# Optimization experiments

Hardware: AMD Instinct MI355X
Metric: run time of the kernel (lower is better)

## Reference

```python
import jax, jax.numpy as jnp
import numpy as np

EPS = 1e-12  # F.normalize eps

def _l2norm(x):
    n = jnp.linalg.norm(x, axis=-1, keepdims=True)
    return x / jnp.maximum(n, EPS)

def setup_inputs() -> dict:
    key = jax.random.key(0)
    k1, k2, k3, k4 = jax.random.split(key, 4)
    N, D = 16384, 256
    img = jax.random.normal(k1, (N, D), dtype=jnp.float32)
    txt = jax.random.normal(k2, (N, D), dtype=jnp.float32)
    t_prime = jax.random.normal(k3, (), dtype=jnp.float32)
    bias = jax.random.normal(k4, (), dtype=jnp.float32)
    return {"img": img, "txt": txt, "t_prime": t_prime, "bias": bias}

def reference(img, txt, t_prime, bias):
    # world_size == 1 path of DistributedSigLoss.forward
    n = img.shape[0]
    image_features = _l2norm(img)
    text_features = _l2norm(txt)
    # logits = exp(t') * img @ txt.T + b   -> [N, N]
    logits = jnp.exp(t_prime) * (image_features @ text_features.T) + bias
    # labels = 2*I - 1 (positive pairs on the diagonal, negatives elsewhere)
    labels = 2.0 * jnp.eye(n, dtype=logits.dtype) - 1.0
    loss = -jnp.sum(jax.nn.log_sigmoid(labels * logits)) / n
    return loss
```

## Files before the change

### kernel.cpp

```cpp
#include <hip/hip_runtime.h>

typedef int   i32x4 __attribute__((ext_vector_type(4)));
typedef int   i32x8 __attribute__((ext_vector_type(8)));
typedef float f32x16 __attribute__((ext_vector_type(16)));

#define D_DIM 256
#define LOG2E 1.4426950408889634f
#define LN2   0.6931471805599453f
#define STRIP_BYTES 32768
#define NBLK 16384

#if __has_builtin(__builtin_amdgcn_exp2f)
static __device__ __forceinline__ float exp2_fast(float x) { return __builtin_amdgcn_exp2f(x); }
#else
static __device__ __forceinline__ float exp2_fast(float x) { return __expf(x * LN2); }
#endif
#if __has_builtin(__builtin_amdgcn_logf)
static __device__ __forceinline__ float log2_fast(float x) { return __builtin_amdgcn_logf(x); }
#else
static __device__ __forceinline__ float log2_fast(float x) { return __logf(x) * LOG2E; }
#endif

#if __has_builtin(__builtin_amdgcn_cvt_pk_fp8_f32)
static __device__ __forceinline__ unsigned int pack4_fp8(float a, float b, float c, float d) {
    int v = 0;
    v = __builtin_amdgcn_cvt_pk_fp8_f32(a, b, v, false);
    v = __builtin_amdgcn_cvt_pk_fp8_f32(c, d, v, true);
    return (unsigned int)v;
}
#else
#include <hip/hip_fp8.h>
static __device__ __forceinline__ unsigned char cv1(float x) {
    __hip_fp8_e4m3 f(x);
    union { __hip_fp8_e4m3 f; unsigned char b; } u; u.f = f; return u.b;
}
static __device__ __forceinline__ unsigned int pack4_fp8(float a, float b, float c, float d) {
    return (unsigned int)cv1(a) | ((unsigned int)cv1(b) << 8) |
           ((unsigned int)cv1(c) << 16) | ((unsigned int)cv1(d) << 24);
}
#endif

static __device__ __forceinline__ f32x16 mfma_fp8_32x32_k64(i32x8 a, i32x8 b, f32x16 c) {
#if __has_builtin(__builtin_amdgcn_mfma_scale_f32_32x32x64_f8f6f4)
    return __builtin_amdgcn_mfma_scale_f32_32x32x64_f8f6f4(a, b, c, 0, 0, 0, 127, 0, 127);
#else
    union { i32x8 v; long l[4]; } ua, ub;
    ua.v = a; ub.v = b;
#pragma unroll
    for (int s = 0; s < 4; ++s)
        c = __builtin_amdgcn_mfma_f32_32x32x16_fp8_fp8(ua.l[s], ub.l[s], c, 0, 0, 0);
    return c;
#endif
}

__global__ __launch_bounds__(256) void norm_cast_kernel(
    const float* __restrict__ img, const float* __restrict__ txt,
    unsigned char* __restrict__ Ab, unsigned char* __restrict__ Bb, int N)
{
    const int tid = threadIdx.x;
    const int q   = tid & 3;
    const int rl  = tid >> 2;
    int gRow = blockIdx.x * 64 + rl;

    const float* src;
    unsigned char* dstB;
    int row;
    if (gRow < N) { row = gRow;     src = img + (size_t)row * D_DIM; dstB = Ab; }
    else          { row = gRow - N; src = txt + (size_t)row * D_DIM; dstB = Bb; }

    float f[64];
    float ss = 0.0f;
    const float4* s4 = (const float4*)(src + q * 64);
#pragma unroll
    for (int i = 0; i < 16; ++i) {
        float4 v = s4[i];
        f[4*i+0] = v.x; f[4*i+1] = v.y; f[4*i+2] = v.z; f[4*i+3] = v.w;
        ss += v.x*v.x + v.y*v.y + v.z*v.z + v.w*v.w;
    }
    ss += __shfl_xor(ss, 1, 64);
    ss += __shfl_xor(ss, 2, 64);
    float inv = 1.0f / fmaxf(sqrtf(ss), 1e-12f);

    unsigned char* dst = dstB + (size_t)(row >> 7) * STRIP_BYTES + (row & 127) * 16;
#pragma unroll
    for (int g = 0; g < 4; ++g) {
        const float* h = f + g * 16;
        uint4 w;
        w.x = pack4_fp8(h[ 0]*inv, h[ 1]*inv, h[ 2]*inv, h[ 3]*inv);
        w.y = pack4_fp8(h[ 4]*inv, h[ 5]*inv, h[ 6]*inv, h[ 7]*inv);
        w.z = pack4_fp8(h[ 8]*inv, h[ 9]*inv, h[10]*inv, h[11]*inv);
        w.w = pack4_fp8(h[12]*inv, h[13]*inv, h[14]*inv, h[15]*inv);
        *(uint4*)(dst + (q * 4 + g) * 2048) = w;
    }
}

__global__ __launch_bounds__(256, 4) void siglip_loss_kernel(
    const unsigned char* __restrict__ A, const unsigned char* __restrict__ B,
    const float* __restrict__ t_prime, const float* __restrict__ bias,
    float* __restrict__ partials, int N)
{
    __shared__ unsigned char As[2][8192];
    __shared__ unsigned char Bs[2][8192];
    __shared__ float red[4];

    const int tid  = threadIdx.x;
    const int wave = tid >> 6;
    const int lane = tid & 63;
    const int r31  = lane & 31;
    const int g    = lane >> 5;
    const int wv   = wave >> 1;
    const int wu   = wave & 1;

    const int bid = blockIdx.x;
    const int st  = bid >> 8;
    const int l2  = bid & 255;
    const int bx  = (st & 7) * 16 + (l2 & 15);
    const int by  = (st >> 3) * 16 + (l2 >> 4);
    const int rowBase = by * 128;
    const int colBase = bx * 128;

    const unsigned char* Astrip = A + (size_t)by * STRIP_BYTES;
    const unsigned char* Bstrip = B + (size_t)bx * STRIP_BYTES;

    auto stage = [&](int buf, int c) {
        const unsigned char* ga = Astrip + c * 8192;
        const unsigned char* gb = Bstrip + c * 8192;
#pragma unroll
        for (int l = 0; l < 2; ++l) {
            int idx = wave * 2 + l;
            __builtin_amdgcn_global_load_lds(
                (const __attribute__((address_space(1))) unsigned int*)(ga + idx * 1024 + lane * 16),
                (__attribute__((address_space(3))) unsigned int*)&As[buf][idx * 1024],
                16, 0, 0);
            __builtin_amdgcn_global_load_lds(
                (const __attribute__((address_space(1))) unsigned int*)(gb + idx * 1024 + lane * 16),
                (__attribute__((address_space(3))) unsigned int*)&Bs[buf][idx * 1024],
                16, 0, 0);
        }
    };

    stage(0, 0);

    int a_off[2], b_off[2];
#pragma unroll
    for (int i = 0; i < 2; ++i) a_off[i] = g * 4096 + (wv * 64 + i * 32 + r31) * 16;
#pragma unroll
    for (int j = 0; j < 2; ++j) b_off[j] = g * 4096 + (wu * 64 + j * 32 + r31) * 16;

    f32x16 acc[2][2] = {};
    union F { i32x8 v8; i32x4 v4[2]; };

#pragma unroll 1
    for (int c = 0; c < 4; ++c) {
        __syncthreads();
        if (c < 3) stage((c + 1) & 1, c + 1);

        const unsigned char* as = As[c & 1];
        const unsigned char* bs = Bs[c & 1];
        F a[2], b[2];
#pragma unroll
        for (int i = 0; i < 2; ++i) {
            a[i].v4[0] = *(const i32x4*)&as[a_off[i]];
            a[i].v4[1] = *(const i32x4*)&as[a_off[i] + 2048];
            b[i].v4[0] = *(const i32x4*)&bs[b_off[i]];
            b[i].v4[1] = *(const i32x4*)&bs[b_off[i] + 2048];
        }
#pragma unroll
        for (int i = 0; i < 2; ++i)
#pragma unroll
            for (int j = 0; j < 2; ++j)
                acc[i][j] = mfma_fp8_32x32_k64(a[i].v8, b[j].v8, acc[i][j]);
    }

    const float s2 = __expf(t_prime[0]) * LOG2E;
    const float b2 = bias[0] * LOG2E;
    float local = 0.0f;
#pragma unroll
    for (int i = 0; i < 2; ++i)
#pragma unroll
        for (int j = 0; j < 2; ++j)
#pragma unroll
            for (int g2 = 0; g2 < 2; ++g2) {
                float x[8];
#pragma unroll
                for (int e = 0; e < 8; ++e)
                    x[e] = exp2_fast(fmaf(s2, acc[i][j][g2 * 8 + e], b2));
                float p = 1.0f + x[0];
#pragma unroll
                for (int e = 1; e < 8; ++e)
                    p = fmaf(p, x[e], p);
                local += log2_fast(p);
            }

    if (rowBase == colBase) {
#pragma unroll
        for (int i = 0; i < 2; ++i)
#pragma unroll
            for (int j = 0; j < 2; ++j)
#pragma unroll
                for (int r = 0; r < 16; ++r) {
                    int rowf = (r & 3) + 8 * (r >> 2) + 4 * g;
                    int grow = wv * 64 + i * 32 + rowf;
                    int gcol = wu * 64 + j * 32 + r31;
                    if (grow == gcol) local -= fmaf(s2, acc[i][j][r], b2);
                }
    }

#pragma unroll
    for (int off = 32; off > 0; off >>= 1)
        local += __shfl_xor(local, off, 64);
    if (lane == 0) red[wave] = local;
    __syncthreads();
    if (tid == 0)
        partials[bid] = (red[0] + red[1]) + (red[2] + red[3]);
}

__global__ __launch_bounds__(1024) void reduce_kernel(
    const float* __restrict__ partials, float* __restrict__ out, int N)
{
    __shared__ float red[16];
    const int tid  = threadIdx.x;
    const int wave = tid >> 6;
    const int lane = tid & 63;
    float s = 0.0f;
#pragma unroll 4
    for (int i = tid; i < NBLK; i += 1024)
        s += partials[i];
#pragma unroll
    for (int off = 32; off > 0; off >>= 1)
        s += __shfl_xor(s, off, 64);
    if (lane == 0) red[wave] = s;
    __syncthreads();
    if (tid == 0) {
        float t = 0.0f;
#pragma unroll
        for (int w = 0; w < 16; ++w) t += red[w];
        out[0] = t * (LN2 / (float)N);
    }
}

extern "C" void kernel_launch(void* const* d_in, const int* in_sizes, int n_in,
                              void* d_out, int out_size, void* d_ws, size_t ws_size,
                              hipStream_t stream) {
    const float* img = (const float*)d_in[0];
    const float* txt = (const float*)d_in[1];
    const float* tp  = (const float*)d_in[2];
    const float* bs  = (const float*)d_in[3];
    float* out = (float*)d_out;
    int N = in_sizes[0] / D_DIM;

    unsigned char* Ab = (unsigned char*)d_ws;
    unsigned char* Bb = Ab + (size_t)N * D_DIM;
    float* partials   = (float*)(Bb + (size_t)N * D_DIM);

    norm_cast_kernel<<<(2 * N) / 64, 256, 0, stream>>>(img, txt, Ab, Bb, N);
    siglip_loss_kernel<<<NBLK, 256, 0, stream>>>(Ab, Bb, tp, bs, partials, N);
    reduce_kernel<<<1, 1024, 0, stream>>>(partials, out, N);
}
```

Baseline: 180.2 us.

## Fuse final reduction via last-block atomic counter; one wave per row in norm kernel

Drops the separate reduce kernel. Each loss block now bumps a global atomic counter after writing its partial, and the last block to finish sums all partials and writes the output. The counter is reset inside the norm kernel. The norm kernel is also restructured to one wave per row with a full-wave shuffle reduction and 4-byte stores, which gives more parallelism but smaller, scattered writes. This saves one kernel launch and its tail latency, at the cost of an atomic plus fence in every loss block.

Result: slower. 442.6 us (+145.6%).

```diff
diff --git a/kernel.cpp b/kernel.cpp
--- a/kernel.cpp
+++ b/kernel.cpp
@@ -55,12 +55,14 @@
 
 __global__ __launch_bounds__(256) void norm_cast_kernel(
     const float* __restrict__ img, const float* __restrict__ txt,
-    unsigned char* __restrict__ Ab, unsigned char* __restrict__ Bb, int N)
+    unsigned char* __restrict__ Ab, unsigned char* __restrict__ Bb,
+    unsigned int* __restrict__ counter, int N)
 {
-    const int tid = threadIdx.x;
-    const int q   = tid & 3;
-    const int rl  = tid >> 2;
-    int gRow = blockIdx.x * 64 + rl;
+    if (blockIdx.x == 0 && threadIdx.x == 0) *counter = 0u;
+
+    const int wave = threadIdx.x >> 6;
+    const int lane = threadIdx.x & 63;
+    int gRow = blockIdx.x * 4 + wave;
 
     const float* src;
     unsigned char* dstB;
@@ -68,40 +70,29 @@
     if (gRow < N) { row = gRow;     src = img + (size_t)row * D_DIM; dstB = Ab; }
     else          { row = gRow - N; src = txt + (size_t)row * D_DIM; dstB = Bb; }
 
-    float f[64];
-    float ss = 0.0f;
-    const float4* s4 = (const float4*)(src + q * 64);
-#pragma unroll
-    for (int i = 0; i < 16; ++i) {
-        float4 v = s4[i];
-        f[4*i+0] = v.x; f[4*i+1] = v.y; f[4*i+2] = v.z; f[4*i+3] = v.w;
-        ss += v.x*v.x + v.y*v.y + v.z*v.z + v.w*v.w;
-    }
-    ss += __shfl_xor(ss, 1, 64);
-    ss += __shfl_xor(ss, 2, 64);
+    float4 v = ((const float4*)src)[lane];
+    float ss = v.x*v.x + v.y*v.y + v.z*v.z + v.w*v.w;
+#pragma unroll
+    for (int off = 1; off < 64; off <<= 1)
+        ss += __shfl_xor(ss, off, 64);
     float inv = 1.0f / fmaxf(sqrtf(ss), 1e-12f);
 
-    unsigned char* dst = dstB + (size_t)(row >> 7) * STRIP_BYTES + (row & 127) * 16;
-#pragma unroll
-    for (int g = 0; g < 4; ++g) {
-        const float* h = f + g * 16;
-        uint4 w;
-        w.x = pack4_fp8(h[ 0]*inv, h[ 1]*inv, h[ 2]*inv, h[ 3]*inv);
-        w.y = pack4_fp8(h[ 4]*inv, h[ 5]*inv, h[ 6]*inv, h[ 7]*inv);
-        w.z = pack4_fp8(h[ 8]*inv, h[ 9]*inv, h[10]*inv, h[11]*inv);
-        w.w = pack4_fp8(h[12]*inv, h[13]*inv, h[14]*inv, h[15]*inv);
-        *(uint4*)(dst + (q * 4 + g) * 2048) = w;
-    }
+    unsigned int w = pack4_fp8(v.x*inv, v.y*inv, v.z*inv, v.w*inv);
+    unsigned char* dst = dstB + (size_t)(row >> 7) * STRIP_BYTES
+                       + (lane >> 2) * 2048 + (row & 127) * 16 + (lane & 3) * 4;
+    *(unsigned int*)dst = w;
 }
 
 __global__ __launch_bounds__(256, 4) void siglip_loss_kernel(
     const unsigned char* __restrict__ A, const unsigned char* __restrict__ B,
     const float* __restrict__ t_prime, const float* __restrict__ bias,
-    float* __restrict__ partials, int N)
+    float* __restrict__ partials, unsigned int* __restrict__ counter,
+    float* __restrict__ out, int N)
 {
     __shared__ unsigned char As[2][8192];
     __shared__ unsigned char Bs[2][8192];
     __shared__ float red[4];
+    __shared__ int isLast;
 
     const int tid  = threadIdx.x;
     const int wave = tid >> 6;
@@ -211,31 +202,27 @@
         local += __shfl_xor(local, off, 64);
     if (lane == 0) red[wave] = local;
     __syncthreads();
-    if (tid == 0)
+    if (tid == 0) {
         partials[bid] = (red[0] + red[1]) + (red[2] + red[3]);
-}
-
-__global__ __launch_bounds__(1024) void reduce_kernel(
-    const float* __restrict__ partials, float* __restrict__ out, int N)
-{
-    __shared__ float red[16];
-    const int tid  = threadIdx.x;
-    const int wave = tid >> 6;
-    const int lane = tid & 63;
-    float s = 0.0f;
-#pragma unroll 4
-    for (int i = tid; i < NBLK; i += 1024)
-        s += partials[i];
-#pragma unroll
-    for (int off = 32; off > 0; off >>= 1)
-        s += __shfl_xor(s, off, 64);
-    if (lane == 0) red[wave] = s;
+        __threadfence();
+        unsigned int old = atomicAdd(counter, 1u);
+        isLast = (old == (unsigned int)(NBLK - 1)) ? 1 : 0;
+    }
     __syncthreads();
-    if (tid == 0) {
-        float t = 0.0f;
-#pragma unroll
-        for (int w = 0; w < 16; ++w) t += red[w];
-        out[0] = t * (LN2 / (float)N);
+
+    if (isLast) {
+        __threadfence();
+        float s = 0.0f;
+#pragma unroll 8
+        for (int i = tid; i < NBLK; i += 256)
+            s += partials[i];
+#pragma unroll
+        for (int off = 32; off > 0; off >>= 1)
+            s += __shfl_xor(s, off, 64);
+        if (lane == 0) red[wave] = s;
+        __syncthreads();
+        if (tid == 0)
+            out[0] = ((red[0] + red[1]) + (red[2] + red[3])) * (LN2 / (float)N);
     }
 }
 
@@ -252,8 +239,8 @@
     unsigned char* Ab = (unsigned char*)d_ws;
     unsigned char* Bb = Ab + (size_t)N * D_DIM;
     float* partials   = (float*)(Bb + (size_t)N * D_DIM);
-
-    norm_cast_kernel<<<(2 * N) / 64, 256, 0, stream>>>(img, txt, Ab, Bb, N);
-    siglip_loss_kernel<<<NBLK, 256, 0, stream>>>(Ab, Bb, tp, bs, partials, N);
-    reduce_kernel<<<1, 1024, 0, stream>>>(partials, out, N);
-}
+    unsigned int* counter = (unsigned int*)(partials + NBLK);
+
+    norm_cast_kernel<<<(2 * N) / 4, 256, 0, stream>>>(img, txt, Ab, Bb, counter, N);
+    siglip_loss_kernel<<<NBLK, 256, 0, stream>>>(Ab, Bb, tp, bs, partials, counter, out, N);
+}
```
